# Optimization experiments

Hardware: AMD Instinct MI355X
Metric: run time of the kernel (lower is better)

## Reference

```python
import jax, jax.numpy as jnp
import numpy as np
from jax import lax

DN = ('NHWC', 'HWIO', 'NHWC')
NEG = -1e30  # stand-in for -inf at inactive sites during masked max-pool


def setup_inputs() -> dict:
    key = jax.random.key(0)
    ks = jax.random.split(key, 6)
    B, H, W, Cin = 1024, 21, 21, 200
    x = jax.random.normal(ks[0], (B, H, W, Cin), dtype=jnp.float32)
    mask = jax.random.randint(ks[1], (B, H, W), 0, 2, dtype=jnp.int32)
    W1 = jax.random.normal(ks[2], (2, 2, Cin, 16), dtype=jnp.float32) * 0.05
    W2 = jax.random.normal(ks[3], (5, 5, 16, 32), dtype=jnp.float32) * 0.05
    Wlin = jax.random.normal(ks[4], (32, 2), dtype=jnp.float32) * 0.1
    blin = jax.random.normal(ks[5], (2,), dtype=jnp.float32) * 0.1
    return {"x": x, "mask": mask, "W1": W1, "W2": W2, "Wlin": Wlin, "blin": blin}


def _masked_maxpool(h, m, win, stride):
    # scn.MaxPooling: max over ACTIVE sites in window; output site active iff any input active.
    hm = jnp.where(m > 0, h, NEG)
    out = lax.reduce_window(hm, NEG, lax.max, (1, win, win, 1), (1, stride, stride, 1), 'VALID')
    m_out = lax.reduce_window(m, 0.0, lax.max, (1, win, win, 1), (1, stride, stride, 1), 'VALID')
    return jnp.where(m_out > 0, out, 0.0), m_out


def reference(x, mask, W1, W2, Wlin, blin):
    m = mask.astype(x.dtype)[..., None]          # [B,21,21,1] active-site mask
    h = x * m                                    # inactive sites carry zero features
    # SubmanifoldConvolution(2, 200, 16, filter=2): size-preserving, gathers only
    # active neighbors (zeros elsewhere), outputs only at input active sites.
    h = lax.conv_general_dilated(h, W1, (1, 1), [(0, 1), (0, 1)], dimension_numbers=DN)
    h = h * m                                    # [B,21,21,16]
    # MaxPooling(2, 3, 3): 21 -> 7
    h, m = _masked_maxpool(h, m, 3, 3)
    # Convolution(2, 16, 32, filter=5, stride=1): 7 -> 3; output active iff any
    # active input in receptive field; value = sum over active inputs (== dense conv on masked feats).
    h = lax.conv_general_dilated(h, W2, (1, 1), 'VALID', dimension_numbers=DN)
    m = lax.reduce_window(m, 0.0, lax.max, (1, 5, 5, 1), (1, 1, 1, 1), 'VALID')
    h = h * m                                    # [B,3,3,32]
    # MaxPooling(2, 3, 1): 3 -> 1
    h, m = _masked_maxpool(h, m, 3, 1)           # [B,1,1,32]
    # SparseToDense already dense here; view(-1, 32), Linear(32,2), softmax(dim=1)
    h = h.reshape(-1, 32)
    return jax.nn.softmax(h @ Wlin + blin, axis=-1)   # [B,2]
```

## Files before the change

kernel.cpp:

```cpp
#include <hip/hip_runtime.h>
#include <math.h>


#define NEGINF -1e30f
#define H1_ELEMS (1024 * 441 * 16)
#define WL_ELEMS (1024 * 441)

__global__ __launch_bounds__(256) void compact_kernel(
    const int* __restrict__ mask,
    int* __restrict__ wl,
    int* __restrict__ nact)
{
    __shared__ unsigned short loc[441];
    __shared__ int cnt, base;
    const int b = blockIdx.x;
    const int t = threadIdx.x;
    if (t == 0) cnt = 0;
    __syncthreads();
    for (int p = t; p < 441; p += 256)
        if (mask[b * 441 + p] != 0) loc[atomicAdd(&cnt, 1)] = (unsigned short)p;
    __syncthreads();
    if (t == 0) base = atomicAdd(nact, cnt);
    __syncthreads();
    const int n = cnt, bs = base, off = b * 441;
    for (int k = t; k < n; k += 256) wl[bs + k] = off + loc[k];
}

__global__ __launch_bounds__(256, 4) void conv1_kernel(
    const float* __restrict__ x,
    const int*   __restrict__ mask,
    const float* __restrict__ W1,
    const int*   __restrict__ wl,
    const int*   __restrict__ nact,
    float* __restrict__ h1)
{
    __shared__ float w1s[4 * 200 * 16];

    {
        const float4* __restrict__ wg = (const float4*)W1;
        float4* wd = (float4*)w1s;
        for (int v = threadIdx.x; v < 3200; v += 256) wd[v] = wg[v];
    }
    __syncthreads();

    const int n = *nact;
    const int gtid = blockIdx.x * 256 + threadIdx.x;
    const int gstride = gridDim.x * 256;

    for (int pair = gtid * 2; pair < n; pair += gstride * 2) {
        const int iA = wl[pair];
        const int iB = wl[min(pair + 1, n - 1)];

        const int bA = iA / 441, pA = iA - bA * 441;
        const int bB = iB / 441, pB = iB - bB * 441;
        const int ia = pA / 21, ja = pA - ia * 21;
        const int ib = pB / 21, jb = pB - ib * 21;

        float accA[16], accB[16];
        #pragma unroll
        for (int c = 0; c < 16; ++c) { accA[c] = 0.0f; accB[c] = 0.0f; }

        #pragma unroll
        for (int tap = 0; tap < 4; ++tap) {
            const int di = tap >> 1, dj = tap & 1;

            const int iiA = ia + di, jjA = ja + dj;
            const bool vA = (iiA < 21) & (jjA < 21);
            const int qA = vA ? (iiA * 21 + jjA) : pA;
            const float mA = (vA && mask[bA * 441 + qA] != 0) ? 1.0f : 0.0f;
            const float4* __restrict__ pa = (const float4*)(x + (size_t)(bA * 441 + qA) * 200);

            const int iiB = ib + di, jjB = jb + dj;
            const bool vB = (iiB < 21) & (jjB < 21);
            const int qB = vB ? (iiB * 21 + jjB) : pB;
            const float mB = (vB && mask[bB * 441 + qB] != 0) ? 1.0f : 0.0f;
            const float4* __restrict__ pb = (const float4*)(x + (size_t)(bB * 441 + qB) * 200);

            const float4* wbase = ((const float4*)w1s) + tap * 800;

            #pragma unroll 2
            for (int k4 = 0; k4 < 50; ++k4) {
                float4 xa = pa[k4];
                float4 xb = pb[k4];
                xa.x *= mA; xa.y *= mA; xa.z *= mA; xa.w *= mA;
                xb.x *= mB; xb.y *= mB; xb.z *= mB; xb.w *= mB;
                const float4* wp = wbase + k4 * 16;
                #pragma unroll
                for (int q = 0; q < 4; ++q) {
                    const float xsa = (q == 0) ? xa.x : (q == 1) ? xa.y : (q == 2) ? xa.z : xa.w;
                    const float xsb = (q == 0) ? xb.x : (q == 1) ? xb.y : (q == 2) ? xb.z : xb.w;
                    const float4 w0 = wp[q * 4 + 0];
                    const float4 w1 = wp[q * 4 + 1];
                    const float4 w2 = wp[q * 4 + 2];
                    const float4 w3 = wp[q * 4 + 3];
                    accA[0]  = fmaf(xsa, w0.x, accA[0]);  accB[0]  = fmaf(xsb, w0.x, accB[0]);
                    accA[1]  = fmaf(xsa, w0.y, accA[1]);  accB[1]  = fmaf(xsb, w0.y, accB[1]);
                    accA[2]  = fmaf(xsa, w0.z, accA[2]);  accB[2]  = fmaf(xsb, w0.z, accB[2]);
                    accA[3]  = fmaf(xsa, w0.w, accA[3]);  accB[3]  = fmaf(xsb, w0.w, accB[3]);
                    accA[4]  = fmaf(xsa, w1.x, accA[4]);  accB[4]  = fmaf(xsb, w1.x, accB[4]);
                    accA[5]  = fmaf(xsa, w1.y, accA[5]);  accB[5]  = fmaf(xsb, w1.y, accB[5]);
                    accA[6]  = fmaf(xsa, w1.z, accA[6]);  accB[6]  = fmaf(xsb, w1.z, accB[6]);
                    accA[7]  = fmaf(xsa, w1.w, accA[7]);  accB[7]  = fmaf(xsb, w1.w, accB[7]);
                    accA[8]  = fmaf(xsa, w2.x, accA[8]);  accB[8]  = fmaf(xsb, w2.x, accB[8]);
                    accA[9]  = fmaf(xsa, w2.y, accA[9]);  accB[9]  = fmaf(xsb, w2.y, accB[9]);
                    accA[10] = fmaf(xsa, w2.z, accA[10]); accB[10] = fmaf(xsb, w2.z, accB[10]);
                    accA[11] = fmaf(xsa, w2.w, accA[11]); accB[11] = fmaf(xsb, w2.w, accB[11]);
                    accA[12] = fmaf(xsa, w3.x, accA[12]); accB[12] = fmaf(xsb, w3.x, accB[12]);
                    accA[13] = fmaf(xsa, w3.y, accA[13]); accB[13] = fmaf(xsb, w3.y, accB[13]);
                    accA[14] = fmaf(xsa, w3.z, accA[14]); accB[14] = fmaf(xsb, w3.z, accB[14]);
                    accA[15] = fmaf(xsa, w3.w, accA[15]); accB[15] = fmaf(xsb, w3.w, accB[15]);
                }
            }
        }

        float4* dA = (float4*)(h1 + (size_t)iA * 16);
        dA[0] = make_float4(accA[0],  accA[1],  accA[2],  accA[3]);
        dA[1] = make_float4(accA[4],  accA[5],  accA[6],  accA[7]);
        dA[2] = make_float4(accA[8],  accA[9],  accA[10], accA[11]);
        dA[3] = make_float4(accA[12], accA[13], accA[14], accA[15]);
        float4* dB = (float4*)(h1 + (size_t)iB * 16);
        dB[0] = make_float4(accB[0],  accB[1],  accB[2],  accB[3]);
        dB[1] = make_float4(accB[4],  accB[5],  accB[6],  accB[7]);
        dB[2] = make_float4(accB[8],  accB[9],  accB[10], accB[11]);
        dB[3] = make_float4(accB[12], accB[13], accB[14], accB[15]);
    }
}

__global__ __launch_bounds__(256) void tail_kernel(
    const float* __restrict__ h1,
    const int*   __restrict__ mask,
    const float* __restrict__ W2,
    const float* __restrict__ Wlin,
    const float* __restrict__ blin,
    float* __restrict__ out)
{
    __shared__ float h1s[441][16];
    __shared__ unsigned char msk[441];
    __shared__ float h2s[49][16];
    __shared__ float m2s[49];
    __shared__ float hc[9][32];
    __shared__ float m3s[9];
    __shared__ float h4[32];

    const int b = blockIdx.x;
    const int t = threadIdx.x;

    for (int p = t; p < 441; p += 256) {
        const int mv = mask[b * 441 + p];
        msk[p] = (unsigned char)(mv != 0);
        if (mv != 0) {
            const float4* __restrict__ src = (const float4*)(h1 + (size_t)(b * 441 + p) * 16);
            float4* dst = (float4*)&h1s[p][0];
            dst[0] = src[0]; dst[1] = src[1]; dst[2] = src[2]; dst[3] = src[3];
        }
    }
    __syncthreads();

    for (int t2 = t; t2 < 784; t2 += 256) {
        const int cell = t2 >> 4;
        const int ch   = t2 & 15;
        const int pr = cell / 7, pc = cell - pr * 7;
        float best = NEGINF;
        bool any = false;
        #pragma unroll
        for (int r = 0; r < 3; ++r) {
            #pragma unroll
            for (int c = 0; c < 3; ++c) {
                const int s = (pr * 3 + r) * 21 + (pc * 3 + c);
                if (msk[s]) { any = true; best = fmaxf(best, h1s[s][ch]); }
            }
        }
        h2s[cell][ch] = any ? best : 0.0f;
        if (ch == 0) m2s[cell] = any ? 1.0f : 0.0f;
    }
    __syncthreads();

    for (int t2 = t; t2 < 288; t2 += 256) {
        const int cell = t2 >> 5;
        const int oc   = t2 & 31;
        const int ci = cell / 3, cj = cell - ci * 3;
        float acc = 0.0f;
        float mm = 0.0f;
        #pragma unroll
        for (int di = 0; di < 5; ++di) {
            #pragma unroll
            for (int dj = 0; dj < 5; ++dj) {
                const int s = (ci + di) * 7 + (cj + dj);
                mm = fmaxf(mm, m2s[s]);
                const float* __restrict__ wrow = W2 + ((di * 5 + dj) * 16) * 32 + oc;
                #pragma unroll
                for (int c = 0; c < 16; ++c)
                    acc = fmaf(h2s[s][c], wrow[c * 32], acc);
            }
        }
        hc[cell][oc] = (mm > 0.0f) ? acc : 0.0f;
        if (oc == 0) m3s[cell] = mm;
    }
    __syncthreads();

    if (t < 32) {
        float best = NEGINF;
        bool any = false;
        #pragma unroll
        for (int cell = 0; cell < 9; ++cell) {
            if (m3s[cell] > 0.0f) { any = true; best = fmaxf(best, hc[cell][t]); }
        }
        h4[t] = any ? best : 0.0f;
    }
    __syncthreads();

    if (t == 0) {
        float l0 = blin[0], l1 = blin[1];
        #pragma unroll
        for (int c = 0; c < 32; ++c) {
            l0 = fmaf(h4[c], Wlin[c * 2 + 0], l0);
            l1 = fmaf(h4[c], Wlin[c * 2 + 1], l1);
        }
        const float mx = fmaxf(l0, l1);
        const float e0 = expf(l0 - mx);
        const float e1 = expf(l1 - mx);
        const float inv = 1.0f / (e0 + e1);
        out[b * 2 + 0] = e0 * inv;
        out[b * 2 + 1] = e1 * inv;
    }
}

extern "C" void kernel_launch(void* const* d_in, const int* in_sizes, int n_in,
                              void* d_out, int out_size, void* d_ws, size_t ws_size,
                              hipStream_t stream) {
    const float* x    = (const float*)d_in[0];
    const int*   mask = (const int*)d_in[1];
    const float* W1   = (const float*)d_in[2];
    const float* W2   = (const float*)d_in[3];
    const float* Wlin = (const float*)d_in[4];
    const float* blin = (const float*)d_in[5];
    float* out = (float*)d_out;

    float* h1   = (float*)d_ws;
    int*   wl   = (int*)(h1 + H1_ELEMS);
    int*   nact = wl + WL_ELEMS;

    hipMemsetAsync(nact, 0, sizeof(int), stream);
    compact_kernel<<<1024, 256, 0, stream>>>(mask, wl, nact);
    conv1_kernel<<<512, 256, 0, stream>>>(x, mask, W1, wl, nact, h1);
    tail_kernel<<<1024, 256, 0, stream>>>(h1, mask, W2, Wlin, blin, out);
}
```

Baseline: 762.5 us.

## Fuse first max-pool into conv1 via ordered-int atomicMax, prefetch input taps

Conv1 results are no longer written to a full-resolution h1 buffer. Each active site instead folds its 16 channels into the pooled 7x7 cell with atomicMax on an order-preserving int encoding of the float. The compact kernel initialises the pooled buffer and computes the pooled mask, and the tail kernel now reads the small pooled tensor directly. Conv1 also interleaves all four taps per k-chunk, uses a software-prefetched register buffer, and points inactive neighbours at a zero page so it skips the mask multiplies. In exchange it adds atomic contention and higher register pressure (launch bounds lowered to 3 blocks per SM).

```diff
diff --git a/kernel.cpp b/kernel.cpp
--- a/kernel.cpp
+++ b/kernel.cpp
@@ -3,39 +3,62 @@
 
 
 #define NEGINF -1e30f
-#define H1_ELEMS (1024 * 441 * 16)
-#define WL_ELEMS (1024 * 441)
+
+__device__ __forceinline__ int f2o(float f) {
+    int i = __float_as_int(f);
+    return (i >= 0) ? i : (i ^ 0x7FFFFFFF);
+}
+__device__ __forceinline__ float o2f(int o) {
+    return __int_as_float((o >= 0) ? o : (o ^ 0x7FFFFFFF));
+}
 
 __global__ __launch_bounds__(256) void compact_kernel(
     const int* __restrict__ mask,
     int* __restrict__ wl,
-    int* __restrict__ nact)
+    int* __restrict__ nact,
+    int* __restrict__ h2ord,
+    float* __restrict__ m2)
 {
     __shared__ unsigned short loc[441];
+    __shared__ unsigned char msk[441];
     __shared__ int cnt, base;
     const int b = blockIdx.x;
     const int t = threadIdx.x;
     if (t == 0) cnt = 0;
     __syncthreads();
-    for (int p = t; p < 441; p += 256)
-        if (mask[b * 441 + p] != 0) loc[atomicAdd(&cnt, 1)] = (unsigned short)p;
+    for (int p = t; p < 441; p += 256) {
+        const int mv = mask[b * 441 + p];
+        msk[p] = (unsigned char)(mv != 0);
+        if (mv != 0) loc[atomicAdd(&cnt, 1)] = (unsigned short)p;
+    }
+    for (int v = t; v < 784; v += 256) h2ord[b * 784 + v] = 0x80000000;
     __syncthreads();
     if (t == 0) base = atomicAdd(nact, cnt);
     __syncthreads();
     const int n = cnt, bs = base, off = b * 441;
     for (int k = t; k < n; k += 256) wl[bs + k] = off + loc[k];
-}
-
-__global__ __launch_bounds__(256, 4) void conv1_kernel(
+    if (t < 49) {
+        const int pr = t / 7, pc = t - pr * 7;
+        int any = 0;
+        #pragma unroll
+        for (int r = 0; r < 3; ++r) {
+            const unsigned char* mr = &msk[(pr * 3 + r) * 21 + pc * 3];
+            any |= mr[0] | mr[1] | mr[2];
+        }
+        m2[b * 49 + t] = any ? 1.0f : 0.0f;
+    }
+}
+
+__global__ __launch_bounds__(256, 3) void conv1_kernel(
     const float* __restrict__ x,
     const int*   __restrict__ mask,
     const float* __restrict__ W1,
     const int*   __restrict__ wl,
     const int*   __restrict__ nact,
-    float* __restrict__ h1)
+    const float* __restrict__ zp,
+    int* __restrict__ h2ord)
 {
     __shared__ float w1s[4 * 200 * 16];
-
     {
         const float4* __restrict__ wg = (const float4*)W1;
         float4* wd = (float4*)w1s;
@@ -44,98 +67,117 @@
     __syncthreads();
 
     const int n = *nact;
+    if (n == 0) return;
+    const int npairs = (n + 1) >> 1;
     const int gtid = blockIdx.x * 256 + threadIdx.x;
     const int gstride = gridDim.x * 256;
 
-    for (int pair = gtid * 2; pair < n; pair += gstride * 2) {
-        const int iA = wl[pair];
-        const int iB = wl[min(pair + 1, n - 1)];
-
+    for (int pr_ = gtid; pr_ < npairs; pr_ += gstride) {
+        const int iA = wl[pr_ * 2];
+        const int iB = wl[min(pr_ * 2 + 1, n - 1)];
         const int bA = iA / 441, pA = iA - bA * 441;
         const int bB = iB / 441, pB = iB - bB * 441;
         const int ia = pA / 21, ja = pA - ia * 21;
         const int ib = pB / 21, jb = pB - ib * 21;
 
-        float accA[16], accB[16];
-        #pragma unroll
-        for (int c = 0; c < 16; ++c) { accA[c] = 0.0f; accB[c] = 0.0f; }
-
+        const float4* pa[4];
+        const float4* pb[4];
         #pragma unroll
         for (int tap = 0; tap < 4; ++tap) {
             const int di = tap >> 1, dj = tap & 1;
-
-            const int iiA = ia + di, jjA = ja + dj;
-            const bool vA = (iiA < 21) & (jjA < 21);
-            const int qA = vA ? (iiA * 21 + jjA) : pA;
-            const float mA = (vA && mask[bA * 441 + qA] != 0) ? 1.0f : 0.0f;
-            const float4* __restrict__ pa = (const float4*)(x + (size_t)(bA * 441 + qA) * 200);
-
-            const int iiB = ib + di, jjB = jb + dj;
-            const bool vB = (iiB < 21) & (jjB < 21);
-            const int qB = vB ? (iiB * 21 + jjB) : pB;
-            const float mB = (vB && mask[bB * 441 + qB] != 0) ? 1.0f : 0.0f;
-            const float4* __restrict__ pb = (const float4*)(x + (size_t)(bB * 441 + qB) * 200);
-
-            const float4* wbase = ((const float4*)w1s) + tap * 800;
-
-            #pragma unroll 2
-            for (int k4 = 0; k4 < 50; ++k4) {
-                float4 xa = pa[k4];
-                float4 xb = pb[k4];
-                xa.x *= mA; xa.y *= mA; xa.z *= mA; xa.w *= mA;
-                xb.x *= mB; xb.y *= mB; xb.z *= mB; xb.w *= mB;
-                const float4* wp = wbase + k4 * 16;
+            {
+                const int ii = ia + di, jj = ja + dj;
+                const bool v = (ii < 21) && (jj < 21);
+                const int q = ii * 21 + jj;
+                pa[tap] = (v && mask[bA * 441 + q] != 0)
+                        ? (const float4*)(x + ((size_t)bA * 441 + q) * 200)
+                        : (const float4*)zp;
+            }
+            {
+                const int ii = ib + di, jj = jb + dj;
+                const bool v = (ii < 21) && (jj < 21);
+                const int q = ii * 21 + jj;
+                pb[tap] = (v && mask[bB * 441 + q] != 0)
+                        ? (const float4*)(x + ((size_t)bB * 441 + q) * 200)
+                        : (const float4*)zp;
+            }
+        }
+
+        float accA[16], accB[16];
+        #pragma unroll
+        for (int c = 0; c < 16; ++c) { accA[c] = 0.0f; accB[c] = 0.0f; }
+
+        float4 cur[8];
+        #pragma unroll
+        for (int tap = 0; tap < 4; ++tap) { cur[tap] = pa[tap][0]; cur[4 + tap] = pb[tap][0]; }
+
+        for (int k4 = 0; k4 < 50; ++k4) {
+            float4 nxt[8];
+            const int kn = (k4 < 49) ? (k4 + 1) : 49;
+            #pragma unroll
+            for (int tap = 0; tap < 4; ++tap) {
+                nxt[tap]     = pa[tap][kn];
+                nxt[4 + tap] = pb[tap][kn];
+            }
+
+            #pragma unroll
+            for (int tap = 0; tap < 4; ++tap) {
+                const float4 xa = cur[tap];
+                const float4 xb = cur[4 + tap];
+                const float4* wt = (const float4*)(w1s + tap * 3200 + k4 * 64);
                 #pragma unroll
                 for (int q = 0; q < 4; ++q) {
                     const float xsa = (q == 0) ? xa.x : (q == 1) ? xa.y : (q == 2) ? xa.z : xa.w;
                     const float xsb = (q == 0) ? xb.x : (q == 1) ? xb.y : (q == 2) ? xb.z : xb.w;
-                    const float4 w0 = wp[q * 4 + 0];
-                    const float4 w1 = wp[q * 4 + 1];
-                    const float4 w2 = wp[q * 4 + 2];
-                    const float4 w3 = wp[q * 4 + 3];
-                    accA[0]  = fmaf(xsa, w0.x, accA[0]);  accB[0]  = fmaf(xsb, w0.x, accB[0]);
-                    accA[1]  = fmaf(xsa, w0.y, accA[1]);  accB[1]  = fmaf(xsb, w0.y, accB[1]);
-                    accA[2]  = fmaf(xsa, w0.z, accA[2]);  accB[2]  = fmaf(xsb, w0.z, accB[2]);
-                    accA[3]  = fmaf(xsa, w0.w, accA[3]);  accB[3]  = fmaf(xsb, w0.w, accB[3]);
-                    accA[4]  = fmaf(xsa, w1.x, accA[4]);  accB[4]  = fmaf(xsb, w1.x, accB[4]);
-                    accA[5]  = fmaf(xsa, w1.y, accA[5]);  accB[5]  = fmaf(xsb, w1.y, accB[5]);
-                    accA[6]  = fmaf(xsa, w1.z, accA[6]);  accB[6]  = fmaf(xsb, w1.z, accB[6]);
-                    accA[7]  = fmaf(xsa, w1.w, accA[7]);  accB[7]  = fmaf(xsb, w1.w, accB[7]);
-                    accA[8]  = fmaf(xsa, w2.x, accA[8]);  accB[8]  = fmaf(xsb, w2.x, accB[8]);
-                    accA[9]  = fmaf(xsa, w2.y, accA[9]);  accB[9]  = fmaf(xsb, w2.y, accB[9]);
-                    accA[10] = fmaf(xsa, w2.z, accA[10]); accB[10] = fmaf(xsb, w2.z, accB[10]);
-                    accA[11] = fmaf(xsa, w2.w, accA[11]); accB[11] = fmaf(xsb, w2.w, accB[11]);
-                    accA[12] = fmaf(xsa, w3.x, accA[12]); accB[12] = fmaf(xsb, w3.x, accB[12]);
-                    accA[13] = fmaf(xsa, w3.y, accA[13]); accB[13] = fmaf(xsb, w3.y, accB[13]);
-                    accA[14] = fmaf(xsa, w3.z, accA[14]); accB[14] = fmaf(xsb, w3.z, accB[14]);
-                    accA[15] = fmaf(xsa, w3.w, accA[15]); accB[15] = fmaf(xsb, w3.w, accB[15]);
+                    const float4 w0 = wt[q * 4 + 0];
+                    const float4 w1v = wt[q * 4 + 1];
+                    const float4 w2v = wt[q * 4 + 2];
+                    const float4 w3v = wt[q * 4 + 3];
+                    accA[0]  = fmaf(xsa, w0.x,  accA[0]);  accB[0]  = fmaf(xsb, w0.x,  accB[0]);
+                    accA[1]  = fmaf(xsa, w0.y,  accA[1]);  accB[1]  = fmaf(xsb, w0.y,  accB[1]);
+                    accA[2]  = fmaf(xsa, w0.z,  accA[2]);  accB[2]  = fmaf(xsb, w0.z,  accB[2]);
+                    accA[3]  = fmaf(xsa, w0.w,  accA[3]);  accB[3]  = fmaf(xsb, w0.w,  accB[3]);
+                    accA[4]  = fmaf(xsa, w1v.x, accA[4]);  accB[4]  = fmaf(xsb, w1v.x, accB[4]);
+                    accA[5]  = fmaf(xsa, w1v.y, accA[5]);  accB[5]  = fmaf(xsb, w1v.y, accB[5]);
+                    accA[6]  = fmaf(xsa, w1v.z, accA[6]);  accB[6]  = fmaf(xsb, w1v.z, accB[6]);
+                    accA[7]  = fmaf(xsa, w1v.w, accA[7]);  accB[7]  = fmaf(xsb, w1v.w, accB[7]);
+                    accA[8]  = fmaf(xsa, w2v.x, accA[8]);  accB[8]  = fmaf(xsb, w2v.x, accB[8]);
+                    accA[9]  = fmaf(xsa, w2v.y, accA[9]);  accB[9]  = fmaf(xsb, w2v.y, accB[9]);
+                    accA[10] = fmaf(xsa, w2v.z, accA[10]); accB[10] = fmaf(xsb, w2v.z, accB[10]);
+                    accA[11] = fmaf(xsa, w2v.w, accA[11]); accB[11] = fmaf(xsb, w2v.w, accB[11]);
+                    accA[12] = fmaf(xsa, w3v.x, accA[12]); accB[12] = fmaf(xsb, w3v.x, accB[12]);
+                    accA[13] = fmaf(xsa, w3v.y, accA[13]); accB[13] = fmaf(xsb, w3v.y, accB[13]);
+                    accA[14] = fmaf(xsa, w3v.z, accA[14]); accB[14] = fmaf(xsb, w3v.z, accB[14]);
+                    accA[15] = fmaf(xsa, w3v.w, accA[15]); accB[15] = fmaf(xsb, w3v.w, accB[15]);
                 }
             }
-        }
-
-        float4* dA = (float4*)(h1 + (size_t)iA * 16);
-        dA[0] = make_float4(accA[0],  accA[1],  accA[2],  accA[3]);
-        dA[1] = make_float4(accA[4],  accA[5],  accA[6],  accA[7]);
-        dA[2] = make_float4(accA[8],  accA[9],  accA[10], accA[11]);
-        dA[3] = make_float4(accA[12], accA[13], accA[14], accA[15]);
-        float4* dB = (float4*)(h1 + (size_t)iB * 16);
-        dB[0] = make_float4(accB[0],  accB[1],  accB[2],  accB[3]);
-        dB[1] = make_float4(accB[4],  accB[5],  accB[6],  accB[7]);
-        dB[2] = make_float4(accB[8],  accB[9],  accB[10], accB[11]);
-        dB[3] = make_float4(accB[12], accB[13], accB[14], accB[15]);
+            #pragma unroll
+            for (int u = 0; u < 8; ++u) cur[u] = nxt[u];
+        }
+
+        {
+            const int cellA = (ia / 3) * 7 + (ja / 3);
+            int* d = h2ord + ((size_t)bA * 49 + cellA) * 16;
+            #pragma unroll
+            for (int c = 0; c < 16; ++c) atomicMax(&d[c], f2o(accA[c]));
+        }
+        {
+            const int cellB = (ib / 3) * 7 + (jb / 3);
+            int* d = h2ord + ((size_t)bB * 49 + cellB) * 16;
+            #pragma unroll
+            for (int c = 0; c < 16; ++c) atomicMax(&d[c], f2o(accB[c]));
+        }
     }
 }
 
 __global__ __launch_bounds__(256) void tail_kernel(
-    const float* __restrict__ h1,
-    const int*   __restrict__ mask,
+    const int*   __restrict__ h2ord,
+    const float* __restrict__ m2,
     const float* __restrict__ W2,
     const float* __restrict__ Wlin,
     const float* __restrict__ blin,
     float* __restrict__ out)
 {
-    __shared__ float h1s[441][16];
-    __shared__ unsigned char msk[441];
     __shared__ float h2s[49][16];
     __shared__ float m2s[49];
     __shared__ float hc[9][32];
@@ -145,33 +187,13 @@
     const int b = blockIdx.x;
     const int t = threadIdx.x;
 
-    for (int p = t; p < 441; p += 256) {
-        const int mv = mask[b * 441 + p];
-        msk[p] = (unsigned char)(mv != 0);
-        if (mv != 0) {
-            const float4* __restrict__ src = (const float4*)(h1 + (size_t)(b * 441 + p) * 16);
-            float4* dst = (float4*)&h1s[p][0];
-            dst[0] = src[0]; dst[1] = src[1]; dst[2] = src[2]; dst[3] = src[3];
-        }
-    }
-    __syncthreads();
-
-    for (int t2 = t; t2 < 784; t2 += 256) {
-        const int cell = t2 >> 4;
-        const int ch   = t2 & 15;
-        const int pr = cell / 7, pc = cell - pr * 7;
-        float best = NEGINF;
-        bool any = false;
-        #pragma unroll
-        for (int r = 0; r < 3; ++r) {
-            #pragma unroll
-            for (int c = 0; c < 3; ++c) {
-                const int s = (pr * 3 + r) * 21 + (pc * 3 + c);
-                if (msk[s]) { any = true; best = fmaxf(best, h1s[s][ch]); }
-            }
-        }
-        h2s[cell][ch] = any ? best : 0.0f;
-        if (ch == 0) m2s[cell] = any ? 1.0f : 0.0f;
+    if (t < 49) m2s[t] = m2[b * 49 + t];
+    __syncthreads();
+
+    for (int v = t; v < 784; v += 256) {
+        const int cell = v >> 4;
+        const int o = h2ord[b * 784 + v];
+        h2s[cell][v & 15] = (m2s[cell] > 0.0f) ? o2f(o) : 0.0f;
     }
     __syncthreads();
 
@@ -236,12 +258,15 @@
     const float* blin = (const float*)d_in[5];
     float* out = (float*)d_out;
 
-    float* h1   = (float*)d_ws;
-    int*   wl   = (int*)(h1 + H1_ELEMS);
-    int*   nact = wl + WL_ELEMS;
+    int*   h2ord = (int*)d_ws;
+    float* m2    = (float*)(h2ord + 1024 * 49 * 16);
+    int*   wl    = (int*)(m2 + 1024 * 49);
+    int*   nact  = wl + 1024 * 441;
+    float* zp    = (float*)(nact + 4);
 
     hipMemsetAsync(nact, 0, sizeof(int), stream);
-    compact_kernel<<<1024, 256, 0, stream>>>(mask, wl, nact);
-    conv1_kernel<<<512, 256, 0, stream>>>(x, mask, W1, wl, nact, h1);
-    tail_kernel<<<1024, 256, 0, stream>>>(h1, mask, W2, Wlin, blin, out);
-}
+    hipMemsetAsync(zp, 0, 256 * sizeof(float), stream);
+    compact_kernel<<<1024, 256, 0, stream>>>(mask, wl, nact, h2ord, m2);
+    conv1_kernel<<<512, 256, 0, stream>>>(x, mask, W1, wl, nact, zp, h2ord);
+    tail_kernel<<<1024, 256, 0, stream>>>(h2ord, m2, W2, Wlin, blin, out);
+}
```

New measurement: 822.7 us. 1.08x slower.
